# Kernel optimization log

Hardware: AMD Instinct MI355X
Metric: run time of the kernel (lower is better)

## Reference

```python
import jax, jax.numpy as jnp
import numpy as np

H = 16          # query heads
HKV = 4         # kv heads
DK = 128        # head_qk_dim
DV = 128        # head_v_dim
HID = 2048
KSZ = 4         # conv kernel size
EPS = 1e-5
NORMALIZER = 16.0


def _causal_dwconv_silu(x, w):
    # x: (B,S,C), w: (C,K). Causal depthwise conv then SiLU.
    B, S, C = x.shape
    K = w.shape[1]
    xp = jnp.pad(x, ((0, 0), (K - 1, 0), (0, 0)))
    y = jnp.zeros_like(x)
    for i in range(K):  # K=4, tiny fixed loop
        y = y + w[:, i] * xp[:, i:i + S, :]
    return jax.nn.silu(y)


def _l2norm(x, eps=1e-6):
    return x * jax.lax.rsqrt(jnp.sum(x * x, axis=-1, keepdims=True) + eps)


def setup_inputs() -> dict:
    key = jax.random.key(0)
    ks = jax.random.split(key, 8)
    B, S = 2, 2048
    qkv_dim = H * DK + HKV * DK + HKV * DV  # 3072
    s = lambda fan_in: 1.0 / np.sqrt(fan_in)
    return {
        "hidden_states": jax.random.normal(ks[0], (B, S, HID), jnp.float32),
        "qkv_w": jax.random.uniform(ks[1], (qkv_dim, HID), jnp.float32, -s(HID), s(HID)),
        "g_w": jax.random.uniform(ks[2], (H * DV, HID), jnp.float32, -s(HID), s(HID)),
        "b_w": jax.random.uniform(ks[3], (H, HID), jnp.float32, -s(HID), s(HID)),
        "gk_w": jax.random.uniform(ks[4], (H, HID), jnp.float32, -s(HID), s(HID)),
        "conv_w": jax.random.uniform(ks[5], (qkv_dim, KSZ), jnp.float32, -s(KSZ), s(KSZ)),
        "out_norm_w": jnp.ones((DV,), jnp.float32),
        "o_w": jax.random.uniform(ks[6], (HID, H * DV), jnp.float32, -s(H * DV), s(H * DV)),
    }


def reference(hidden_states, qkv_w, g_w, b_w, gk_w, conv_w, out_norm_w, o_w):
    x = hidden_states
    B, S, _ = x.shape
    grp = H // HKV

    qkv = x @ qkv_w.T                                   # (B,S,3072)
    qkv = _causal_dwconv_silu(qkv, conv_w)
    q, k, v = jnp.split(qkv, [H * DK, H * DK + HKV * DK], axis=-1)
    q = q.reshape(B, S, H, DK)
    k = k.reshape(B, S, HKV, DK)
    v = v.reshape(B, S, HKV, DV)
    # GQA expansion
    k = jnp.repeat(k, grp, axis=2)                      # (B,S,H,DK)
    v = jnp.repeat(v, grp, axis=2)                      # (B,S,H,DV)

    # q/k L2 norm + scale
    q = _l2norm(q) * (DK ** -0.5)
    k = _l2norm(k)

    # decay gate (logsigmoid, log-space), write strength beta
    g_log = jax.nn.log_sigmoid(x @ gk_w.T) / NORMALIZER  # (B,S,H)
    alpha = jnp.exp(g_log)
    beta = jax.nn.sigmoid(x @ b_w.T)                     # (B,S,H)

    # gated delta rule: S_t = a_t*S_{t-1} + k_t (x) beta_t*(v_t - k_t @ (a_t*S_{t-1}))
    def step(Sstate, inp):
        q_t, k_t, v_t, a_t, b_t = inp                    # (B,H,*)
        Sstate = Sstate * a_t[..., None, None]           # (B,H,DK,DV)
        v_pred = jnp.einsum('bhk,bhkv->bhv', k_t, Sstate)
        delta = (v_t - v_pred) * b_t[..., None]
        Sstate = Sstate + jnp.einsum('bhk,bhv->bhkv', k_t, delta)
        o_t = jnp.einsum('bhk,bhkv->bhv', q_t, Sstate)
        return Sstate, o_t

    tfirst = lambda a: jnp.moveaxis(a, 1, 0)             # (S,B,H,...)
    S0 = jnp.zeros((B, H, DK, DV), x.dtype)
    _, o = jax.lax.scan(step, S0, (tfirst(q), tfirst(k), tfirst(v), tfirst(alpha), tfirst(beta)))
    o = jnp.moveaxis(o, 0, 1)                            # (B,S,H,DV)

    # gated per-head RMSNorm then output projection
    g = (x @ g_w.T).reshape(B, S, H, DV)
    o = o * jax.lax.rsqrt(jnp.mean(o * o, axis=-1, keepdims=True) + EPS) * out_norm_w
    o = o * jax.nn.silu(g)
    return (o.reshape(B, S, H * DV)) @ o_w.T
```

## Files before the change

kernel.cpp:

```cpp
#include <hip/hip_runtime.h>
#include <math.h>

#define S_LEN 2048
#define BATCH 2
#define NH 16
#define NKV 4
#define DKQ 128
#define DVV 128
#define HID 2048
#define QKV_DIM 3072
#define M_TOK 4096

typedef _Float16 halfx8 __attribute__((ext_vector_type(8)));
typedef _Float16 halfx4 __attribute__((ext_vector_type(4)));
typedef float floatx4 __attribute__((ext_vector_type(4)));

#define AS1 __attribute__((address_space(1)))
#define AS3 __attribute__((address_space(3)))
#define GLD16(gp, lp) __builtin_amdgcn_global_load_lds((AS1 const void*)(gp), (AS3 void*)(lp), 16, 0, 0)
#define MFMA16(a, b, c) __builtin_amdgcn_mfma_f32_16x16x32_f16(a, b, c, 0, 0, 0)
#define SBAR() asm volatile("s_barrier" ::: "memory")

#define PA_STRIDE 81920

__device__ __forceinline__ float sigmoidf_(float x) { return 1.f / (1.f + __expf(-x)); }

__global__ __launch_bounds__(256) void cvt_f16(const float* __restrict__ in,
                                               _Float16* __restrict__ out, int n8) {
  int i = blockIdx.x * 256 + threadIdx.x;
  if (i >= n8) return;
  const float4* p = (const float4*)in;
  float4 a = p[2 * (size_t)i], b = p[2 * (size_t)i + 1];
  halfx8 o;
  o[0] = (_Float16)a.x; o[1] = (_Float16)a.y; o[2] = (_Float16)a.z; o[3] = (_Float16)a.w;
  o[4] = (_Float16)b.x; o[5] = (_Float16)b.y; o[6] = (_Float16)b.z; o[7] = (_Float16)b.w;
  *(halfx8*)(out + (size_t)i * 8) = o;
}

__global__ __launch_bounds__(512, 2) void gemm_bt_f16_4ph(const _Float16* __restrict__ A,
                                                          const _Float16* __restrict__ B,
                                                          float* __restrict__ C,
                                                          int M, int N, int K) {
  __shared__ char lds[98304] __attribute__((aligned(16)));
  const int tid = threadIdx.x;
  const int wid = tid >> 6, l = tid & 63;
  const int lr = l & 15, hi = l >> 4;
  const int wm = wid & 3, wn = wid >> 2;

  int nbx = gridDim.x;
  int bid = blockIdx.y * nbx + blockIdx.x;
  int nwg = nbx * gridDim.y;
  int swz = (nwg & 7) ? bid : ((bid & 7) * (nwg >> 3) + (bid >> 3));
  int bm = (swz / nbx) * 256, bn = (swz % nbx) * 128;

  const int srow = wid * 8 + (l >> 3);
  const int csrc = ((l & 7) ^ (l >> 3)) * 8;
  const _Float16* ga[4];
  const _Float16* gb[2];
#pragma unroll
  for (int q = 0; q < 4; ++q) ga[q] = A + (size_t)(bm + q * 64 + srow) * K + csrc;
#pragma unroll
  for (int q = 0; q < 2; ++q) gb[q] = B + (size_t)(bn + q * 64 + srow) * K + csrc;
  int soff[6];
#pragma unroll
  for (int q = 0; q < 4; ++q) soff[q] = q * 8192 + (wid << 10);
#pragma unroll
  for (int q = 0; q < 2; ++q) soff[4 + q] = 32768 + q * 8192 + (wid << 10);

  int cr[2];
  cr[0] = (hi ^ (lr & 7)) * 16;
  cr[1] = ((4 + hi) ^ (lr & 7)) * 16;
  const int abase = wm * 8192 + lr * 128;
  const int bbase = 32768 + wn * 8192 + lr * 128;

  floatx4 acc[4][4];
#pragma unroll
  for (int i = 0; i < 4; ++i)
#pragma unroll
    for (int j = 0; j < 4; ++j) acc[i][j] = (floatx4){0.f, 0.f, 0.f, 0.f};

  const int NT = K >> 6;
#define STAGE6(tt, pp)                                           \
  {                                                              \
    int kof = (tt) * 64;                                         \
    int pof = (pp) * 49152;                                      \
    _Pragma("unroll") for (int q = 0; q < 4; ++q)                \
        GLD16(ga[q] + kof, lds + pof + soff[q]);                 \
    _Pragma("unroll") for (int q = 0; q < 2; ++q)                \
        GLD16(gb[q] + kof, lds + pof + soff[4 + q]);             \
  }

  STAGE6(0, 0);
  asm volatile("s_waitcnt vmcnt(0)" ::: "memory");
  SBAR();

  halfx8 af[2][2], bf[4][2];
  for (int t = 0; t < NT; ++t) {
    const char* bufc = lds + (t & 1) * 49152;
    if (t + 1 < NT) STAGE6(t + 1, (t + 1) & 1);
#pragma unroll
    for (int mi = 0; mi < 2; ++mi)
#pragma unroll
      for (int ks = 0; ks < 2; ++ks)
        af[mi][ks] = *(const halfx8*)(bufc + abase + mi * 2048 + cr[ks]);
#pragma unroll
    for (int ni = 0; ni < 2; ++ni)
#pragma unroll
      for (int ks = 0; ks < 2; ++ks)
        bf[ni][ks] = *(const halfx8*)(bufc + bbase + ni * 2048 + cr[ks]);
    SBAR();
    __builtin_amdgcn_s_setprio(1);
#pragma unroll
    for (int mi = 0; mi < 2; ++mi)
#pragma unroll
      for (int ni = 0; ni < 2; ++ni)
#pragma unroll
        for (int ks = 0; ks < 2; ++ks)
          acc[mi][ni] = MFMA16(af[mi][ks], bf[ni][ks], acc[mi][ni]);
    __builtin_amdgcn_s_setprio(0);
    SBAR();
#pragma unroll
    for (int ni = 2; ni < 4; ++ni)
#pragma unroll
      for (int ks = 0; ks < 2; ++ks)
        bf[ni][ks] = *(const halfx8*)(bufc + bbase + ni * 2048 + cr[ks]);
    SBAR();
    __builtin_amdgcn_s_setprio(1);
#pragma unroll
    for (int mi = 0; mi < 2; ++mi)
#pragma unroll
      for (int ni = 2; ni < 4; ++ni)
#pragma unroll
        for (int ks = 0; ks < 2; ++ks)
          acc[mi][ni] = MFMA16(af[mi][ks], bf[ni][ks], acc[mi][ni]);
    __builtin_amdgcn_s_setprio(0);
    SBAR();
#pragma unroll
    for (int mi = 0; mi < 2; ++mi)
#pragma unroll
      for (int ks = 0; ks < 2; ++ks)
        af[mi][ks] = *(const halfx8*)(bufc + abase + (mi + 2) * 2048 + cr[ks]);
    SBAR();
    __builtin_amdgcn_s_setprio(1);
#pragma unroll
    for (int mi = 0; mi < 2; ++mi)
#pragma unroll
      for (int ni = 2; ni < 4; ++ni)
#pragma unroll
        for (int ks = 0; ks < 2; ++ks)
          acc[mi + 2][ni] = MFMA16(af[mi][ks], bf[ni][ks], acc[mi + 2][ni]);
    __builtin_amdgcn_s_setprio(0);
    SBAR();
    __builtin_amdgcn_s_setprio(1);
#pragma unroll
    for (int mi = 0; mi < 2; ++mi)
#pragma unroll
      for (int ni = 0; ni < 2; ++ni)
#pragma unroll
        for (int ks = 0; ks < 2; ++ks)
          acc[mi + 2][ni] = MFMA16(af[mi][ks], bf[ni][ks], acc[mi + 2][ni]);
    __builtin_amdgcn_s_setprio(0);
    asm volatile("s_waitcnt vmcnt(0)" ::: "memory");
    SBAR();
  }
#pragma unroll
  for (int mi = 0; mi < 4; ++mi)
#pragma unroll
    for (int ni = 0; ni < 4; ++ni) {
      int row0 = bm + wm * 64 + mi * 16 + hi * 4;
      int col = bn + wn * 64 + ni * 16 + lr;
#pragma unroll
      for (int r = 0; r < 4; ++r)
        C[(size_t)(row0 + r) * N + col] = acc[mi][ni][r];
    }
#undef STAGE6
}

__global__ __launch_bounds__(256) void gkb_kernel(const float* __restrict__ X,
                                                  const float* __restrict__ gk_w,
                                                  const float* __restrict__ b_w,
                                                  float* __restrict__ glog,
                                                  float* __restrict__ be) {
  __shared__ float xs[16][260];
  __shared__ float ws[32][260];
  int tid = threadIdx.x;
  int m0 = blockIdx.x * 16;
  int tl = tid >> 4, n0 = tid & 15;
  float acc0 = 0.f, acc1 = 0.f;
  for (int k0 = 0; k0 < HID; k0 += 256) {
#pragma unroll
    for (int i = 0; i < 4; ++i) {
      int F = i * 256 + tid;
      int r = F >> 6, c4 = (F & 63) * 4;
      *(float4*)&xs[r][c4] = *(const float4*)&X[(size_t)(m0 + r) * HID + k0 + c4];
    }
#pragma unroll
    for (int i = 0; i < 8; ++i) {
      int F = i * 256 + tid;
      int r = F >> 6, c4 = (F & 63) * 4;
      const float* src = (r < 16) ? (gk_w + (size_t)r * HID) : (b_w + (size_t)(r - 16) * HID);
      *(float4*)&ws[r][c4] = *(const float4*)&src[k0 + c4];
    }
    __syncthreads();
#pragma unroll 16
    for (int k = 0; k < 256; k += 4) {
      float4 a = *(const float4*)&xs[tl][k];
      float4 w0 = *(const float4*)&ws[n0][k];
      float4 w1 = *(const float4*)&ws[n0 + 16][k];
      acc0 += a.x * w0.x + a.y * w0.y + a.z * w0.z + a.w * w0.w;
      acc1 += a.x * w1.x + a.y * w1.y + a.z * w1.z + a.w * w1.w;
    }
    __syncthreads();
  }
  int m = m0 + tl, b = m >> 11, s = m & (S_LEN - 1);
  float z = acc0;
  float ls = (z >= 0.f) ? -log1pf(expf(-z)) : (z - log1pf(expf(z)));
  size_t oi = (size_t)(b * NH + n0) * S_LEN + s;
  glog[oi] = ls * 0.0625f;
  be[oi] = sigmoidf_(acc1);
}

__global__ __launch_bounds__(256) void conv_kernel(const float* __restrict__ qkv,
                                                   const float* __restrict__ conv_w,
                                                   float* __restrict__ qn,
                                                   float* __restrict__ kn,
                                                   float* __restrict__ vn) {
  __shared__ float ys[QKV_DIM];
  __shared__ float sc[20];
  int m = blockIdx.x;
  int b = m >> 11, s = m & (S_LEN - 1);
  int tid = threadIdx.x;
  for (int c = tid; c < QKV_DIM; c += 256) {
    float acc = 0.f;
#pragma unroll
    for (int i = 0; i < 4; ++i) {
      int si = s - 3 + i;
      if (si >= 0) acc += conv_w[c * 4 + i] * qkv[(size_t)(b * S_LEN + si) * QKV_DIM + c];
    }
    ys[c] = acc * (1.f / (1.f + __expf(-acc)));
  }
  __syncthreads();
  int wv = tid >> 6, lane = tid & 63;
  for (int ch = wv; ch < 20; ch += 4) {
    int base = (ch < 16) ? ch * 128 : 2048 + (ch - 16) * 128;
    float x0 = ys[base + lane], x1 = ys[base + 64 + lane];
    float ss = x0 * x0 + x1 * x1;
#pragma unroll
    for (int off = 1; off < 64; off <<= 1) ss += __shfl_xor(ss, off);
    float scale = rsqrtf(ss + 1e-6f);
    if (ch < 16) scale *= 0.08838834764831845f;
    if (lane == 0) sc[ch] = scale;
  }
  __syncthreads();
  for (int c = tid; c < 2048; c += 256) {
    int h = c >> 7, d = c & 127;
    qn[((size_t)(b * NH + h) * S_LEN + s) * DKQ + d] = ys[c] * sc[h];
  }
  for (int c = tid; c < 512; c += 256) {
    int j = c >> 7, d = c & 127;
    kn[((size_t)(b * NKV + j) * S_LEN + s) * DKQ + d] = ys[2048 + c] * sc[16 + j];
    vn[((size_t)(b * NKV + j) * S_LEN + s) * DVV + d] = ys[2560 + c];
  }
}

__global__ __launch_bounds__(256, 2) void phaseA_kernel(const float* __restrict__ qn,
                                                        const float* __restrict__ kn,
                                                        const float* __restrict__ vn,
                                                        const float* __restrict__ glog,
                                                        const float* __restrict__ be,
                                                        char* __restrict__ pout,
                                                        float* __restrict__ obuf) {
  __shared__ char smem[80128] __attribute__((aligned(16)));
  _Float16* kh = (_Float16*)smem;
  _Float16* qh = (_Float16*)(smem + 22528);
  float*    LT = (float*)(smem + 45056);
  _Float16* Ph = (_Float16*)(smem + 67584);
  float*    sc_c    = (float*)(smem + 78848);
  float*    sc_beta = sc_c + 64;
  float*    sc_gam  = sc_c + 128;
  float*    sc_bg   = sc_c + 192;
  float*    sc_gcr  = sc_c + 256;
  _Float16* Dt = (_Float16*)smem;
  _Float16* Wt = (_Float16*)(smem + 22528);
  _Float16* Kt = (_Float16*)(smem + 45056);

  int u = blockIdx.x;
  int bh = u >> 5, ch = u & 31;
  int t0 = ch * 64;
  int b = bh >> 4, h = bh & 15, kvh = h >> 2;
  const float* qb = qn + ((size_t)bh * S_LEN + t0) * DKQ;
  const float* kb = kn + (((size_t)(b * NKV + kvh)) * S_LEN + t0) * DKQ;
  const float* vb = vn + (((size_t)(b * NKV + kvh)) * S_LEN + t0) * DVV;
  const float* gl = glog + (size_t)bh * S_LEN + t0;
  const float* ber = be + (size_t)bh * S_LEN + t0;
  char* base = pout + (size_t)u * PA_STRIDE;
  _Float16* M_out = (_Float16*)base;
  _Float16* E_out = (_Float16*)(base + 32768);
  _Float16* B_out = (_Float16*)(base + 49152);
  float* ob = obuf + ((size_t)bh * S_LEN + t0) * DVV;

  int tid = threadIdx.x;
  if (tid < 64) {
    float x = gl[tid];
#pragma unroll
    for (int off = 1; off < 64; off <<= 1) {
      float y = __shfl_up(x, off);
      if (tid >= off) x += y;
    }
    sc_c[tid] = x;
  }
#pragma unroll
  for (int i = 0; i < 8; ++i) {
    int idx = i * 256 + tid;
    int t = idx >> 5, d4 = (idx & 31) * 4;
    float4 kv4 = *(const float4*)&kb[(size_t)t * DKQ + d4];
    float4 qv4 = *(const float4*)&qb[(size_t)t * DKQ + d4];
    _Float16* kd = &kh[t * 152 + d4];
    kd[0] = (_Float16)kv4.x; kd[1] = (_Float16)kv4.y; kd[2] = (_Float16)kv4.z; kd[3] = (_Float16)kv4.w;
    _Float16* qd = &qh[t * 152 + d4];
    qd[0] = (_Float16)qv4.x; qd[1] = (_Float16)qv4.y; qd[2] = (_Float16)qv4.z; qd[3] = (_Float16)qv4.w;
  }
  __syncthreads();
  if (tid < 64) {
    float c = sc_c[tid], c63 = sc_c[63];
    float gam = __expf(c);
    float bet = ber[tid];
    sc_gam[tid] = gam; sc_beta[tid] = bet; sc_bg[tid] = bet * gam;
    sc_gcr[tid] = __expf(c63 - c);
  }
  __syncthreads();

  float z[64];
  {
    const float* src = (tid < 128) ? vb : kb;
    const float* mult = (tid < 128) ? sc_beta : sc_bg;
    int col = tid & 127;
#pragma unroll
    for (int t = 0; t < 64; ++t) z[t] = mult[t] * src[(size_t)t * 128 + col];
  }

  int w = tid >> 6, l = tid & 63;
  int lr = l & 15, lk8 = (l >> 4) * 8, q4 = (l >> 4) * 4;
  floatx4 acc[8];
#pragma unroll
  for (int i = 0; i < 8; ++i) acc[i] = (floatx4){0.f, 0.f, 0.f, 0.f};
#pragma unroll
  for (int job = 0; job < 8; ++job) {
    int j2 = w * 8 + job;
    int tm = (j2 & 15) >> 2, tn = j2 & 3;
    const _Float16* Ar = (j2 < 16) ? kh : qh;
#pragma unroll
    for (int kk = 0; kk < 4; ++kk) {
      halfx8 af = *(const halfx8*)&Ar[(tm * 16 + lr) * 152 + kk * 32 + lk8];
      halfx8 bf = *(const halfx8*)&kh[(tn * 16 + lr) * 152 + kk * 32 + lk8];
      acc[job] = MFMA16(af, bf, acc[job]);
    }
  }
#pragma unroll
  for (int job = 0; job < 8; ++job) {
    int j2 = w * 8 + job;
    int tm = (j2 & 15) >> 2, tn = j2 & 3;
    int jcol = tn * 16 + lr;
    float cj = sc_c[jcol];
#pragma unroll
    for (int r = 0; r < 4; ++r) {
      int trow = tm * 16 + q4 + r;
      float val = acc[job][r] * __expf(sc_c[trow] - cj);
      if (j2 < 16) {
        LT[jcol * 68 + trow] = (jcol < trow) ? sc_beta[trow] * val : 0.f;
      } else {
        Ph[trow * 88 + jcol] = (_Float16)((jcol <= trow) ? val : 0.f);
      }
    }
  }
  __syncthreads();

#pragma unroll
  for (int t = 0; t < 64; ++t) {
    float zt = z[t];
    const int start = ((t + 1) >> 2) << 2;
#pragma unroll
    for (int t2 = start; t2 < 64; t2 += 4) {
      float4 lv = *(const float4*)&LT[t * 68 + t2];
      z[t2 + 0] -= lv.x * zt;
      z[t2 + 1] -= lv.y * zt;
      z[t2 + 2] -= lv.z * zt;
      z[t2 + 3] -= lv.w * zt;
    }
  }
  floatx4 Eacc[8];
#pragma unroll
  for (int ni = 0; ni < 8; ++ni)
#pragma unroll
    for (int r = 0; r < 4; ++r) {
      int trow = w * 16 + q4 + r;
      Eacc[ni][r] = sc_gam[trow] * (float)qh[trow * 152 + ni * 16 + lr];
    }
  __syncthreads();

  {
    int d = tid >> 1, tb = (tid & 1) * 32;
#pragma unroll
    for (int j = 0; j < 4; ++j) {
      halfx8 kv;
#pragma unroll
      for (int r = 0; r < 8; ++r) {
        int t = tb + j * 8 + r;
        kv[r] = (_Float16)(sc_gcr[t] * (float)kh[t * 152 + d]);
      }
      *(halfx8*)&Kt[d * 88 + tb + j * 8] = kv;
    }
  }
  if (tid >= 128) {
    int col = tid & 127;
#pragma unroll
    for (int t = 0; t < 64; t += 8) {
      halfx8 wv;
#pragma unroll
      for (int r = 0; r < 8; ++r) wv[r] = (_Float16)(-z[t + r]);
      *(halfx8*)&Wt[col * 88 + t] = wv;
    }
  }
  __syncthreads();
  if (tid < 128) {
    int col = tid & 127;
#pragma unroll
    for (int t = 0; t < 64; t += 8) {
      halfx8 dv;
#pragma unroll
      for (int r = 0; r < 8; ++r) dv[r] = (_Float16)z[t + r];
      *(halfx8*)&Dt[col * 88 + t] = dv;
    }
  }
  __syncthreads();

  floatx4 Macc[2][8], Bacc[2][8], Oacc[8];
  float gC = __expf(sc_c[63]);
#pragma unroll
  for (int mi = 0; mi < 2; ++mi)
#pragma unroll
    for (int ni = 0; ni < 8; ++ni) {
#pragma unroll
      for (int r = 0; r < 4; ++r)
        Macc[mi][ni][r] = ((w * 32 + mi * 16 + q4 + r) == (ni * 16 + lr)) ? gC : 0.f;
      Bacc[mi][ni] = (floatx4){0.f, 0.f, 0.f, 0.f};
    }
#pragma unroll
  for (int ni = 0; ni < 8; ++ni) Oacc[ni] = (floatx4){0.f, 0.f, 0.f, 0.f};
#pragma unroll
  for (int ks = 0; ks < 2; ++ks) {
    halfx8 ka0 = *(const halfx8*)&Kt[(w * 32 + lr) * 88 + ks * 32 + lk8];
    halfx8 ka1 = *(const halfx8*)&Kt[(w * 32 + 16 + lr) * 88 + ks * 32 + lk8];
    halfx8 pa = *(const halfx8*)&Ph[(w * 16 + lr) * 88 + ks * 32 + lk8];
#pragma unroll
    for (int ni = 0; ni < 8; ++ni) {
      halfx8 wb = *(const halfx8*)&Wt[(ni * 16 + lr) * 88 + ks * 32 + lk8];
      halfx8 db = *(const halfx8*)&Dt[(ni * 16 + lr) * 88 + ks * 32 + lk8];
      Macc[0][ni] = MFMA16(ka0, wb, Macc[0][ni]);
      Macc[1][ni] = MFMA16(ka1, wb, Macc[1][ni]);
      Bacc[0][ni] = MFMA16(ka0, db, Bacc[0][ni]);
      Bacc[1][ni] = MFMA16(ka1, db, Bacc[1][ni]);
      Eacc[ni] = MFMA16(pa, wb, Eacc[ni]);
      Oacc[ni] = MFMA16(pa, db, Oacc[ni]);
    }
  }
#pragma unroll
  for (int mi = 0; mi < 2; ++mi)
#pragma unroll
    for (int ni = 0; ni < 8; ++ni)
#pragma unroll
      for (int r = 0; r < 4; ++r) {
        int row = w * 32 + mi * 16 + q4 + r;
        M_out[row * 128 + ni * 16 + lr] = (_Float16)Macc[mi][ni][r];
        B_out[ni * 2048 + row * 16 + lr] = (_Float16)Bacc[mi][ni][r];
      }
#pragma unroll
  for (int ni = 0; ni < 8; ++ni)
#pragma unroll
    for (int r = 0; r < 4; ++r) {
      int trow = w * 16 + q4 + r;
      E_out[trow * 128 + ni * 16 + lr] = (_Float16)Eacc[ni][r];
      ob[(size_t)trow * 128 + ni * 16 + lr] = Oacc[ni][r];
    }
}

__global__ __launch_bounds__(256, 1) void phaseB_kernel(const char* __restrict__ pin,
                                                        float* __restrict__ obuf) {
  __shared__ _Float16 Mh[2][128 * 152];
  __shared__ _Float16 Eh[2][64 * 152];
  __shared__ _Float16 St[2][16 * 152];

  int bh = blockIdx.x & 31, vg = blockIdx.x >> 5;
  int tid = threadIdx.x, w = tid >> 6, l = tid & 63;
  int lr = l & 15, lk8 = (l >> 4) * 8, q4 = (l >> 4) * 4;
  const char* ub0 = pin + (size_t)(bh * 32) * PA_STRIDE;
  float* ob_base = obuf + (size_t)bh * S_LEN * DVV + vg * 16;

  float4 Mr[8], Er[4];
  float Bc[2][4], Oc[4], Bn[2][4], On[4];

  {
    const float4* Mg = (const float4*)ub0;
    const float4* Eg = (const float4*)(ub0 + 32768);
    const _Float16* Bg = (const _Float16*)(ub0 + 49152) + vg * 2048;
#pragma unroll
    for (int j = 0; j < 8; ++j) Mr[j] = Mg[j * 256 + tid];
#pragma unroll
    for (int j = 0; j < 4; ++j) Er[j] = Eg[j * 256 + tid];
#pragma unroll
    for (int mi = 0; mi < 2; ++mi)
#pragma unroll
      for (int r = 0; r < 4; ++r)
        Bc[mi][r] = (float)Bg[(w * 32 + mi * 16 + q4 + r) * 16 + lr];
#pragma unroll
    for (int r = 0; r < 4; ++r)
      Oc[r] = ob_base[(size_t)(w * 16 + q4 + r) * DVV + lr];
#pragma unroll
    for (int j = 0; j < 8; ++j) {
      int n = j * 256 + tid;
      *(float4*)&Mh[0][(n >> 4) * 152 + (n & 15) * 8] = Mr[j];
    }
#pragma unroll
    for (int j = 0; j < 4; ++j) {
      int n = j * 256 + tid;
      *(float4*)&Eh[0][(n >> 4) * 152 + (n & 15) * 8] = Er[j];
    }
    halfx4 z4;
    z4[0] = (_Float16)0.f; z4[1] = (_Float16)0.f; z4[2] = (_Float16)0.f; z4[3] = (_Float16)0.f;
#pragma unroll
    for (int mi = 0; mi < 2; ++mi)
      *(halfx4*)&St[0][lr * 152 + w * 32 + mi * 16 + q4] = z4;
  }
  asm volatile("s_waitcnt lgkmcnt(0)" ::: "memory");

  for (int c = 0; c < 32; ++c) {
    __builtin_amdgcn_s_barrier();
    int cur = c & 1, nxt = cur ^ 1;
    bool have = (c + 1) < 32;
    if (have) {
      const char* un = ub0 + (size_t)(c + 1) * PA_STRIDE;
      const float4* Mg = (const float4*)un;
      const float4* Eg = (const float4*)(un + 32768);
      const _Float16* Bg = (const _Float16*)(un + 49152) + vg * 2048;
#pragma unroll
      for (int j = 0; j < 8; ++j) Mr[j] = Mg[j * 256 + tid];
#pragma unroll
      for (int j = 0; j < 4; ++j) Er[j] = Eg[j * 256 + tid];
#pragma unroll
      for (int mi = 0; mi < 2; ++mi)
#pragma unroll
        for (int r = 0; r < 4; ++r)
          Bn[mi][r] = (float)Bg[(w * 32 + mi * 16 + q4 + r) * 16 + lr];
#pragma unroll
      for (int r = 0; r < 4; ++r)
        On[r] = ob_base[(size_t)((c + 1) * 64 + w * 16 + q4 + r) * DVV + lr];
    }
    floatx4 Sn0 = {Bc[0][0], Bc[0][1], Bc[0][2], Bc[0][3]};
    floatx4 Sn1 = {Bc[1][0], Bc[1][1], Bc[1][2], Bc[1][3]};
    floatx4 Oa = {Oc[0], Oc[1], Oc[2], Oc[3]};
#pragma unroll
    for (int ks = 0; ks < 4; ++ks) {
      halfx8 sf = *(const halfx8*)&St[cur][lr * 152 + ks * 32 + lk8];
      halfx8 ma0 = *(const halfx8*)&Mh[cur][(w * 32 + lr) * 152 + ks * 32 + lk8];
      halfx8 ma1 = *(const halfx8*)&Mh[cur][(w * 32 + 16 + lr) * 152 + ks * 32 + lk8];
      halfx8 ea = *(const halfx8*)&Eh[cur][(w * 16 + lr) * 152 + ks * 32 + lk8];
      Sn0 = MFMA16(ma0, sf, Sn0);
      Sn1 = MFMA16(ma1, sf, Sn1);
      Oa = MFMA16(ea, sf, Oa);
    }
    {
      float* obr = ob_base + (size_t)c * 64 * DVV;
#pragma unroll
      for (int r = 0; r < 4; ++r)
        obr[(size_t)(w * 16 + q4 + r) * DVV + lr] = Oa[r];
    }
#pragma unroll
    for (int mi = 0; mi < 2; ++mi) {
      halfx4 sv;
      floatx4 Sm = mi ? Sn1 : Sn0;
#pragma unroll
      for (int r = 0; r < 4; ++r) sv[r] = (_Float16)Sm[r];
      *(halfx4*)&St[nxt][lr * 152 + w * 32 + mi * 16 + q4] = sv;
    }
    if (have) {
#pragma unroll
      for (int j = 0; j < 8; ++j) {
        int n = j * 256 + tid;
        *(float4*)&Mh[nxt][(n >> 4) * 152 + (n & 15) * 8] = Mr[j];
      }
#pragma unroll
      for (int j = 0; j < 4; ++j) {
        int n = j * 256 + tid;
        *(float4*)&Eh[nxt][(n >> 4) * 152 + (n & 15) * 8] = Er[j];
      }
#pragma unroll
      for (int mi = 0; mi < 2; ++mi)
#pragma unroll
        for (int r = 0; r < 4; ++r) Bc[mi][r] = Bn[mi][r];
#pragma unroll
      for (int r = 0; r < 4; ++r) Oc[r] = On[r];
    }
    asm volatile("s_waitcnt lgkmcnt(0)" ::: "memory");
  }
}

__global__ __launch_bounds__(256) void normgate_kernel(const float* __restrict__ o_buf,
                                                       const float* __restrict__ g_buf,
                                                       const float* __restrict__ nw,
                                                       _Float16* __restrict__ og) {
  int gid = blockIdx.x * 4 + (threadIdx.x >> 6);
  int lane = threadIdx.x & 63;
  int m = gid >> 4, h = gid & 15;
  int b = m >> 11, s = m & (S_LEN - 1);
  const float* orow = o_buf + ((size_t)(b * NH + h) * S_LEN + s) * DVV;
  float o0 = orow[lane], o1 = orow[lane + 64];
  float ss = o0 * o0 + o1 * o1;
#pragma unroll
  for (int off = 1; off < 64; off <<= 1) ss += __shfl_xor(ss, off);
  float r = rsqrtf(ss * (1.f / 128.f) + 1e-5f);
  size_t gi = (size_t)m * HID + h * DVV;
  float g0 = g_buf[gi + lane], g1 = g_buf[gi + lane + 64];
  og[gi + lane] = (_Float16)(o0 * r * nw[lane] * (g0 * sigmoidf_(g0)));
  og[gi + lane + 64] = (_Float16)(o1 * r * nw[lane + 64] * (g1 * sigmoidf_(g1)));
}

extern "C" void kernel_launch(void* const* d_in, const int* in_sizes, int n_in,
                              void* d_out, int out_size, void* d_ws, size_t ws_size,
                              hipStream_t stream) {
  const float* X      = (const float*)d_in[0];
  const float* qkv_w  = (const float*)d_in[1];
  const float* g_w    = (const float*)d_in[2];
  const float* b_w    = (const float*)d_in[3];
  const float* gk_w   = (const float*)d_in[4];
  const float* conv_w = (const float*)d_in[5];
  const float* norm_w = (const float*)d_in[6];
  const float* o_w    = (const float*)d_in[7];
  float* out = (float*)d_out;

  char* ws = (char*)d_ws;
  float* qkv_buf   = (float*)(ws);
  float* g_buf     = (float*)(ws);
  _Float16* ow16   = (_Float16*)(ws + 33554432);
  float* glog      = (float*)(ws + 41943040);
  float* be        = (float*)(ws + 42205184);
  float* qn        = (float*)(ws + 50331648);
  float* kn        = (float*)(ws + 83886080);
  float* vn        = (float*)(ws + 92274688);
  _Float16* X16    = (_Float16*)(ws + 100663296);
  _Float16* qw16   = (_Float16*)(ws + 117440512);
  _Float16* gw16   = (_Float16*)(ws + 130023424);
  char*  pA        = (char*)(ws + 100663296);
  _Float16* og16   = (_Float16*)(ws + 100663296);
  float* o_buf     = qn;

  dim3 blk(256);
  dim3 blk512(512);
  cvt_f16<<<dim3(4096), blk, 0, stream>>>(X, X16, 1048576);
  cvt_f16<<<dim3(3072), blk, 0, stream>>>(qkv_w, qw16, 786432);
  cvt_f16<<<dim3(2048), blk, 0, stream>>>(g_w, gw16, 524288);
  gemm_bt_f16_4ph<<<dim3(QKV_DIM / 128, M_TOK / 256), blk512, 0, stream>>>(X16, qw16, qkv_buf, M_TOK, QKV_DIM, HID);
  conv_kernel<<<dim3(M_TOK), blk, 0, stream>>>(qkv_buf, conv_w, qn, kn, vn);
  gkb_kernel<<<dim3(M_TOK / 16), blk, 0, stream>>>(X, gk_w, b_w, glog, be);
  cvt_f16<<<dim3(2048), blk, 0, stream>>>(o_w, ow16, 524288);
  gemm_bt_f16_4ph<<<dim3(HID / 128, M_TOK / 256), blk512, 0, stream>>>(X16, gw16, g_buf, M_TOK, HID, HID);
  phaseA_kernel<<<dim3(1024), blk, 0, stream>>>(qn, kn, vn, glog, be, pA, o_buf);
  phaseB_kernel<<<dim3(256), blk, 0, stream>>>(pA, o_buf);
  normgate_kernel<<<dim3(M_TOK * NH / 4), blk, 0, stream>>>(o_buf, g_buf, norm_w, og16);
  gemm_bt_f16_4ph<<<dim3(HID / 128, M_TOK / 256), blk512, 0, stream>>>(og16, ow16, out, M_TOK, HID, HID);
}
```

Baseline: 490.1 us.

## Shrink GEMM tile to 128x128 with 4 waves and two-phase MFMA schedule

Replaces the 256x128, 8-wave GEMM with a 128x128, 4-wave variant. Each wave now holds all four A fragments and splits the B fragments into two phases, which cuts LDS to 64KB and reduces barriers per k-step. The grid gets twice as many workgroups, which should help fill the CUs for these mid-size GEMMs. In exchange, arithmetic intensity per tile is lower and global loads per FLOP rise.

```diff
diff --git a/kernel.cpp b/kernel.cpp
--- a/kernel.cpp
+++ b/kernel.cpp
@@ -37,41 +37,39 @@
   *(halfx8*)(out + (size_t)i * 8) = o;
 }
 
-__global__ __launch_bounds__(512, 2) void gemm_bt_f16_4ph(const _Float16* __restrict__ A,
+__global__ __launch_bounds__(256, 2) void gemm_bt_f16_2ph(const _Float16* __restrict__ A,
                                                           const _Float16* __restrict__ B,
                                                           float* __restrict__ C,
                                                           int M, int N, int K) {
-  __shared__ char lds[98304] __attribute__((aligned(16)));
+  __shared__ char lds[65536] __attribute__((aligned(16)));
   const int tid = threadIdx.x;
   const int wid = tid >> 6, l = tid & 63;
   const int lr = l & 15, hi = l >> 4;
-  const int wm = wid & 3, wn = wid >> 2;
+  const int wm = wid & 1, wn = wid >> 1;
 
   int nbx = gridDim.x;
   int bid = blockIdx.y * nbx + blockIdx.x;
   int nwg = nbx * gridDim.y;
   int swz = (nwg & 7) ? bid : ((bid & 7) * (nwg >> 3) + (bid >> 3));
-  int bm = (swz / nbx) * 256, bn = (swz % nbx) * 128;
-
-  const int srow = wid * 8 + (l >> 3);
-  const int csrc = ((l & 7) ^ (l >> 3)) * 8;
+  int bm = (swz / nbx) * 128, bn = (swz % nbx) * 128;
+
+  const int srow = tid >> 3;
+  const int csrc = ((tid & 7) ^ ((tid >> 3) & 7)) * 8;
   const _Float16* ga[4];
-  const _Float16* gb[2];
-#pragma unroll
-  for (int q = 0; q < 4; ++q) ga[q] = A + (size_t)(bm + q * 64 + srow) * K + csrc;
-#pragma unroll
-  for (int q = 0; q < 2; ++q) gb[q] = B + (size_t)(bn + q * 64 + srow) * K + csrc;
-  int soff[6];
-#pragma unroll
-  for (int q = 0; q < 4; ++q) soff[q] = q * 8192 + (wid << 10);
-#pragma unroll
-  for (int q = 0; q < 2; ++q) soff[4 + q] = 32768 + q * 8192 + (wid << 10);
+  const _Float16* gb[4];
+#pragma unroll
+  for (int q = 0; q < 4; ++q) {
+    ga[q] = A + (size_t)(bm + q * 32 + srow) * K + csrc;
+    gb[q] = B + (size_t)(bn + q * 32 + srow) * K + csrc;
+  }
+  const int dstA = tid * 16;
+  const int dstB = 16384 + tid * 16;
 
   int cr[2];
   cr[0] = (hi ^ (lr & 7)) * 16;
   cr[1] = ((4 + hi) ^ (lr & 7)) * 16;
   const int abase = wm * 8192 + lr * 128;
-  const int bbase = 32768 + wn * 8192 + lr * 128;
+  const int bbase = 16384 + wn * 8192 + lr * 128;
 
   floatx4 acc[4][4];
 #pragma unroll
@@ -80,26 +78,26 @@
     for (int j = 0; j < 4; ++j) acc[i][j] = (floatx4){0.f, 0.f, 0.f, 0.f};
 
   const int NT = K >> 6;
-#define STAGE6(tt, pp)                                           \
+#define STAGE8(tt, pp)                                           \
   {                                                              \
     int kof = (tt) * 64;                                         \
-    int pof = (pp) * 49152;                                      \
-    _Pragma("unroll") for (int q = 0; q < 4; ++q)                \
-        GLD16(ga[q] + kof, lds + pof + soff[q]);                 \
-    _Pragma("unroll") for (int q = 0; q < 2; ++q)                \
-        GLD16(gb[q] + kof, lds + pof + soff[4 + q]);             \
-  }
-
-  STAGE6(0, 0);
+    int pof = (pp) * 32768;                                      \
+    _Pragma("unroll") for (int q = 0; q < 4; ++q) {              \
+      GLD16(ga[q] + kof, lds + pof + q * 4096 + dstA);           \
+      GLD16(gb[q] + kof, lds + pof + q * 4096 + dstB);           \
+    }                                                            \
+  }
+
+  STAGE8(0, 0);
   asm volatile("s_waitcnt vmcnt(0)" ::: "memory");
   SBAR();
 
-  halfx8 af[2][2], bf[4][2];
+  halfx8 af[4][2], bf[2][2];
   for (int t = 0; t < NT; ++t) {
-    const char* bufc = lds + (t & 1) * 49152;
-    if (t + 1 < NT) STAGE6(t + 1, (t + 1) & 1);
-#pragma unroll
-    for (int mi = 0; mi < 2; ++mi)
+    const char* bufc = lds + (t & 1) * 32768;
+    if (t + 1 < NT) STAGE8(t + 1, (t + 1) & 1);
+#pragma unroll
+    for (int mi = 0; mi < 4; ++mi)
 #pragma unroll
       for (int ks = 0; ks < 2; ++ks)
         af[mi][ks] = *(const halfx8*)(bufc + abase + mi * 2048 + cr[ks]);
@@ -111,7 +109,7 @@
     SBAR();
     __builtin_amdgcn_s_setprio(1);
 #pragma unroll
-    for (int mi = 0; mi < 2; ++mi)
+    for (int mi = 0; mi < 4; ++mi)
 #pragma unroll
       for (int ni = 0; ni < 2; ++ni)
 #pragma unroll
@@ -120,45 +118,19 @@
     __builtin_amdgcn_s_setprio(0);
     SBAR();
 #pragma unroll
-    for (int ni = 2; ni < 4; ++ni)
+    for (int ni = 0; ni < 2; ++ni)
 #pragma unroll
       for (int ks = 0; ks < 2; ++ks)
-        bf[ni][ks] = *(const halfx8*)(bufc + bbase + ni * 2048 + cr[ks]);
+        bf[ni][ks] = *(const halfx8*)(bufc + bbase + (ni + 2) * 2048 + cr[ks]);
     SBAR();
     __builtin_amdgcn_s_setprio(1);
 #pragma unroll
-    for (int mi = 0; mi < 2; ++mi)
-#pragma unroll
-      for (int ni = 2; ni < 4; ++ni)
+    for (int mi = 0; mi < 4; ++mi)
+#pragma unroll
+      for (int ni = 0; ni < 2; ++ni)
 #pragma unroll
         for (int ks = 0; ks < 2; ++ks)
-          acc[mi][ni] = MFMA16(af[mi][ks], bf[ni][ks], acc[mi][ni]);
-    __builtin_amdgcn_s_setprio(0);
-    SBAR();
-#pragma unroll
-    for (int mi = 0; mi < 2; ++mi)
-#pragma unroll
-      for (int ks = 0; ks < 2; ++ks)
-        af[mi][ks] = *(const halfx8*)(bufc + abase + (mi + 2) * 2048 + cr[ks]);
-    SBAR();
-    __builtin_amdgcn_s_setprio(1);
-#pragma unroll
-    for (int mi = 0; mi < 2; ++mi)
-#pragma unroll
-      for (int ni = 2; ni < 4; ++ni)
-#pragma unroll
-        for (int ks = 0; ks < 2; ++ks)
-          acc[mi + 2][ni] = MFMA16(af[mi][ks], bf[ni][ks], acc[mi + 2][ni]);
-    __builtin_amdgcn_s_setprio(0);
-    SBAR();
-    __builtin_amdgcn_s_setprio(1);
-#pragma unroll
-    for (int mi = 0; mi < 2; ++mi)
-#pragma unroll
-      for (int ni = 0; ni < 2; ++ni)
-#pragma unroll
-        for (int ks = 0; ks < 2; ++ks)
-          acc[mi + 2][ni] = MFMA16(af[mi][ks], bf[ni][ks], acc[mi + 2][ni]);
+          acc[mi][ni + 2] = MFMA16(af[mi][ks], bf[ni][ks], acc[mi][ni + 2]);
     __builtin_amdgcn_s_setprio(0);
     asm volatile("s_waitcnt vmcnt(0)" ::: "memory");
     SBAR();
@@ -173,7 +145,7 @@
       for (int r = 0; r < 4; ++r)
         C[(size_t)(row0 + r) * N + col] = acc[mi][ni][r];
     }
-#undef STAGE6
+#undef STAGE8
 }
 
 __global__ __launch_bounds__(256) void gkb_kernel(const float* __restrict__ X,
@@ -654,17 +626,16 @@
   float* o_buf     = qn;
 
   dim3 blk(256);
-  dim3 blk512(512);
   cvt_f16<<<dim3(4096), blk, 0, stream>>>(X, X16, 1048576);
   cvt_f16<<<dim3(3072), blk, 0, stream>>>(qkv_w, qw16, 786432);
   cvt_f16<<<dim3(2048), blk, 0, stream>>>(g_w, gw16, 524288);
-  gemm_bt_f16_4ph<<<dim3(QKV_DIM / 128, M_TOK / 256), blk512, 0, stream>>>(X16, qw16, qkv_buf, M_TOK, QKV_DIM, HID);
+  gemm_bt_f16_2ph<<<dim3(QKV_DIM / 128, M_TOK / 128), blk, 0, stream>>>(X16, qw16, qkv_buf, M_TOK, QKV_DIM, HID);
   conv_kernel<<<dim3(M_TOK), blk, 0, stream>>>(qkv_buf, conv_w, qn, kn, vn);
   gkb_kernel<<<dim3(M_TOK / 16), blk, 0, stream>>>(X, gk_w, b_w, glog, be);
   cvt_f16<<<dim3(2048), blk, 0, stream>>>(o_w, ow16, 524288);
-  gemm_bt_f16_4ph<<<dim3(HID / 128, M_TOK / 256), blk512, 0, stream>>>(X16, gw16, g_buf, M_TOK, HID, HID);
+  gemm_bt_f16_2ph<<<dim3(HID / 128, M_TOK / 128), blk, 0, stream>>>(X16, gw16, g_buf, M_TOK, HID, HID);
   phaseA_kernel<<<dim3(1024), blk, 0, stream>>>(qn, kn, vn, glog, be, pA, o_buf);
   phaseB_kernel<<<dim3(256), blk, 0, stream>>>(pA, o_buf);
   normgate_kernel<<<dim3(M_TOK * NH / 4), blk, 0, stream>>>(o_buf, g_buf, norm_w, og16);
-  gemm_bt_f16_4ph<<<dim3(HID / 128, M_TOK / 256), blk512, 0, stream>>>(og16, ow16, out, M_TOK, HID, HID);
-}
+  gemm_bt_f16_2ph<<<dim3(HID / 128, M_TOK / 128), blk, 0, stream>>>(og16, ow16, out, M_TOK, HID, HID);
+}
```

New measurement: 487.8 us. About the same (-0.5%).
